# Kernel tuning notes

Hardware: AMD Instinct MI355X
Metric: run time of the kernel (lower is better)

The kernel has to match this reference:

```python
import jax, jax.numpy as jnp
import numpy as np

B, S, E, ND = 4, 2048, 1024, 2


def setup_inputs() -> dict:
    key = jax.random.key(0)
    ks = jax.random.split(key, 10)
    def lin_w(k, out_f, in_f):
        return (jax.random.normal(k, (out_f, in_f), jnp.float32) / np.sqrt(in_f).astype(np.float32))
    inp = {}
    inp["x"] = jax.random.normal(ks[0], (B, S, E), jnp.float32)
    inp["tfidf_scores"] = jax.random.uniform(ks[1], (B, S), jnp.float32)
    names = ["q_f", "k_f", "v_f", "q_b", "k_b", "v_b"]
    for i, n in enumerate(names):
        inp["W" + n] = lin_w(ks[2 + i], ND * E, E)
        inp["b" + n] = jnp.zeros((ND * E,), jnp.float32)
    inp["Wo"] = lin_w(ks[8], E, ND * E)
    inp["bo"] = jnp.zeros((E,), jnp.float32)
    return inp


def _proj(x, W, b):
    # Linear(E -> ND*E) then reshape to (B, S, ND, E)
    y = jnp.einsum('bse,fe->bsf', x, W) + b
    return y.reshape(x.shape[0], x.shape[1], ND, E)


def _attend(q, k, v, tfidf):
    # q,k,v: (B, S, ND, E); tfidf: (B, S) weights keys
    scale = 1.0 / jnp.sqrt(jnp.asarray(E, q.dtype))
    scores = jnp.einsum('bsde,btde->bdst', q, k) * scale
    scores = scores * tfidf[:, None, None, :]
    attn = jax.nn.softmax(scores, axis=-1)
    return jnp.einsum('bdst,btde->bsde', attn, v)


def reference(x, tfidf_scores, Wq_f, bq_f, Wk_f, bk_f, Wv_f, bv_f,
              Wq_b, bq_b, Wk_b, bk_b, Wv_b, bv_b, Wo, bo):
    # forward direction
    qf = _proj(x, Wq_f, bq_f)
    kf = _proj(x, Wk_f, bk_f)
    vf = _proj(x, Wv_f, bv_f)
    out_f = _attend(qf, kf, vf, tfidf_scores)
    # backward direction: reversed sequence
    xr = x[:, ::-1]
    tr = tfidf_scores[:, ::-1]
    qb = _proj(xr, Wq_b, bq_b)
    kb = _proj(xr, Wk_b, bk_b)
    vb = _proj(xr, Wv_b, bv_b)
    out_b = _attend(qb, kb, vb, tr)[:, ::-1]
    comb = (out_f + out_b).reshape(x.shape[0], x.shape[1], ND * E)
    return jnp.einsum('bsf,ef->bse', comb, Wo) + bo
```

## Files before the change

### kernel.cpp

```cpp
#include <hip/hip_runtime.h>
#include <hip/hip_bf16.h>
#include <stdint.h>

#define SEQ 2048
#define EMB 1024

typedef __attribute__((ext_vector_type(4))) float f32x4;
typedef __attribute__((ext_vector_type(8))) __bf16 bf16x8v;
typedef __attribute__((ext_vector_type(8))) unsigned short u16x8;
typedef __attribute__((ext_vector_type(4))) unsigned short u16x4;

static __device__ __forceinline__ float bf2f(unsigned short u){
  union { unsigned int i; float f; } v; v.i = ((unsigned int)u) << 16; return v.f;
}
static __device__ __forceinline__ unsigned short f2bf(float f){
  union { float f; unsigned int i; } v; v.f = f;
  unsigned int r = v.i + 0x7FFFu + ((v.i >> 16) & 1u);
  return (unsigned short)(r >> 16);
}

static __device__ __forceinline__ void gload16(const unsigned short* g, unsigned short* l){
  __builtin_amdgcn_global_load_lds(
      (__attribute__((address_space(1))) unsigned int*)(g),
      (__attribute__((address_space(3))) unsigned int*)(l), 16, 0, 0);
}

static __device__ __forceinline__ int xcd_swz(int bid, int nwg){
  int q = nwg >> 3;
  return (bid & 7) * q + (bid >> 3);
}

__global__ __launch_bounds__(256) void k_cvt_bf16(const float* __restrict__ in,
                                                  unsigned short* __restrict__ out, long n4){
  long i = (long)blockIdx.x * 256 + threadIdx.x;
  if (i >= n4) return;
  float4 v = ((const float4*)in)[i];
  u16x4 o; o.x = f2bf(v.x); o.y = f2bf(v.y); o.z = f2bf(v.z); o.w = f2bf(v.w);
  ((u16x4*)out)[i] = o;
}

__global__ __launch_bounds__(256) void k_build_wcat(
    const float* __restrict__ w0, const float* __restrict__ w1,
    const float* __restrict__ w2, const float* __restrict__ w3,
    const float* __restrict__ w4, const float* __restrict__ w5,
    unsigned short* __restrict__ wcat){
  long i = (long)blockIdx.x * 256 + threadIdx.x;
  long g = i * 4;
  int m = (int)(g >> 21);
  const float* src = (m==0)?w0:(m==1)?w1:(m==2)?w2:(m==3)?w3:(m==4)?w4:w5;
  long loc = g & ((1L<<21)-1);
  float4 v = *(const float4*)&src[loc];
  u16x4 o; o.x=f2bf(v.x); o.y=f2bf(v.y); o.z=f2bf(v.z); o.w=f2bf(v.w);
  *(u16x4*)&wcat[g] = o;
}

__global__ __launch_bounds__(256) void k_build_bcat(
    const float* b0, const float* b1, const float* b2,
    const float* b3, const float* b4, const float* b5, float* __restrict__ bcat){
  int i = blockIdx.x * 256 + threadIdx.x;
  int m = i >> 11;
  const float* src = (m==0)?b0:(m==1)?b1:(m==2)?b2:(m==3)?b3:(m==4)?b4:b5;
  bcat[i] = src[i & 2047];
}

#define M_LIN   0
#define M_SCORE 1
#define M_PV    2
#define M_OUT   3

template<int MODE, int BN>
__global__ __launch_bounds__(512, 2)
void gemm8(const unsigned short* __restrict__ A_,
           const unsigned short* __restrict__ B_,
           unsigned short* __restrict__ Cb, float* __restrict__ Cf,
           const float* __restrict__ bias, const float* __restrict__ tfb,
           int ld, int ldc, int tilesN, int accflag)
{
  constexpr int KD  = (MODE==M_PV || MODE==M_OUT) ? 2048 : 1024;
  constexpr int NT  = KD/64;
  constexpr int NREP= BN/64;
  constexpr int NLO = NREP/2;
  constexpr int GB  = BN/64;

  __shared__ __attribute__((aligned(16))) unsigned short As[2][256*64];
  __shared__ __attribute__((aligned(16))) unsigned short Bs[2][BN*64];

  const int tid = threadIdx.x;
  const int lane = tid & 63, wid = tid >> 6;
  const int wr = wid >> 2, wc = wid & 3;

  const int tile = xcd_swz(blockIdx.x, gridDim.x);
  const int tm = tile / tilesN, tn = tile % tilesN;
  const int y  = blockIdx.y;

  const unsigned short *A0 = A_, *B0 = B_;
  unsigned short* Cbp = Cb;
  float* Cfp = Cf;
  const float* trow = nullptr;

  if constexpr (MODE==M_SCORE) {
    const int bl = y >> 1, d = y & 1;
    A0 = A_ + (size_t)bl*SEQ*ld + d*1024;
    B0 = A0 + 2048;
    Cbp = Cb + (size_t)y*SEQ*SEQ;
    trow = tfb + (size_t)bl*SEQ;
  } else if constexpr (MODE==M_PV) {
    A0 = A_ + (size_t)y*SEQ*SEQ;
    B0 = B_ + (size_t)y*EMB*SEQ;
    Cbp = Cb + (size_t)(y>>1)*SEQ*2048 + (y&1)*1024;
  }

  const int sr = tid >> 3, ss = tid & 7;
  const int swz = (ss ^ (sr & 7)) * 8;
  const long tmrow = (long)tm*256, tncol = (long)tn*BN;
  const int lrow = lane & 15, lks = lane >> 4;

  const unsigned short* gA = A0 + (size_t)(tmrow + sr)*ld + swz;
  const unsigned short* gB = B0 + (size_t)(tncol + sr)*ld + swz;

  f32x4 acc[8][NREP];
  #pragma unroll
  for (int m=0;m<8;++m)
    #pragma unroll
    for (int n=0;n<NREP;++n)
      #pragma unroll
      for (int r=0;r<4;++r) acc[m][n][r] = 0.f;

#define STAGE(nb_, t_) { \
    const long ko_ = (long)(t_)*64; \
    _Pragma("unroll") \
    for (int p=0;p<4;++p) \
      gload16(gA + (size_t)(p*64)*ld + ko_, &As[nb_][p*4096 + tid*8]); \
    _Pragma("unroll") \
    for (int p=0;p<GB;++p) \
      gload16(gB + (size_t)(p*64)*ld + ko_, &Bs[nb_][p*4096 + tid*8]); }

#define LDA_F(dst, mh) { \
    _Pragma("unroll") \
    for (int m=0;m<4;++m){ \
      int row_ = (m + 4*(mh))*32 + wr*16 + lrow; \
      _Pragma("unroll") \
      for (int kk=0;kk<2;++kk){ \
        int slot_ = (kk*4 + lks) ^ (row_ & 7); \
        dst[m*2+kk] = *(const bf16x8v*)&As[buf][row_*64 + slot_*8]; \
      } } }

#define LDB_F(dst, nh) { \
    _Pragma("unroll") \
    for (int n=0;n<NLO;++n){ \
      int row_ = (n + NLO*(nh))*64 + wc*16 + lrow; \
      _Pragma("unroll") \
      for (int kk=0;kk<2;++kk){ \
        int slot_ = (kk*4 + lks) ^ (row_ & 7); \
        dst[n*2+kk] = *(const bf16x8v*)&Bs[buf][row_*64 + slot_*8]; \
      } } }

#define MMAC(mh, bfrag, nh) { \
    __builtin_amdgcn_s_setprio(1); \
    _Pragma("unroll") \
    for (int m=0;m<4;++m) \
      _Pragma("unroll") \
      for (int n=0;n<NLO;++n) \
        _Pragma("unroll") \
        for (int kk=0;kk<2;++kk) \
          acc[(mh)*4+m][(nh)*NLO+n] = __builtin_amdgcn_mfma_f32_16x16x32_bf16( \
              aF[m*2+kk], bfrag[n*2+kk], acc[(mh)*4+m][(nh)*NLO+n], 0,0,0); \
    __builtin_amdgcn_s_setprio(0); }

#define TILE_BODY() { \
    bf16x8v aF[8], bL[2*NLO], bH[2*NLO]; \
    LDA_F(aF, 0); \
    LDB_F(bL, 0); \
    MMAC(0, bL, 0); \
    LDB_F(bH, 1); \
    MMAC(0, bH, 1); \
    LDA_F(aF, 1); \
    MMAC(1, bH, 1); \
    MMAC(1, bL, 0); }

  STAGE(0, 0);
  __syncthreads();

  for (int t = 0; t < NT-1; ++t) {
    const int buf = t & 1;
    STAGE(buf ^ 1, t+1);
    TILE_BODY();
    __syncthreads();
  }
  {
    const int buf = (NT-1) & 1;
    TILE_BODY();
  }

  const int rr = (lane >> 4) * 4, cc = lane & 15;
  #pragma unroll
  for (int n=0;n<NREP;++n) {
    const long col = tncol + n*64 + wc*16 + cc;
    float cmul = 1.f, cadd = 0.f;
    if constexpr (MODE==M_SCORE) cmul = 0.03125f * trow[col];
    if constexpr (MODE==M_LIN)   cadd = bias[col];
    if constexpr (MODE==M_OUT)   cadd = bias[col];
    #pragma unroll
    for (int m=0;m<8;++m) {
      const long row = tmrow + m*32 + wr*16 + rr;
      #pragma unroll
      for (int r=0;r<4;++r) {
        float v = acc[m][n][r];
        if constexpr (MODE==M_SCORE) v *= cmul;
        else v += cadd;
        if constexpr (MODE==M_OUT) {
          Cfp[(row + r)*ldc + col] = v;
        } else if constexpr (MODE==M_PV) {
          size_t idx = (row + r)*(size_t)ldc + col;
          float w = v + (accflag ? bf2f(Cbp[idx]) : 0.f);
          Cbp[idx] = f2bf(w);
        } else {
          Cbp[(row + r)*(size_t)ldc + col] = f2bf(v);
        }
      }
    }
  }
#undef STAGE
#undef LDA_F
#undef LDB_F
#undef MMAC
#undef TILE_BODY
}

__global__ __launch_bounds__(256) void k_softmax(unsigned short* __restrict__ Sc){
  long row = blockIdx.x;
  unsigned short* p = Sc + row*SEQ + threadIdx.x*8;
  u16x8 raw = *(const u16x8*)p;
  float v[8]; float mx = -3.0e38f;
  #pragma unroll
  for (int j=0;j<8;++j){ v[j] = bf2f(raw[j]); mx = fmaxf(mx, v[j]); }
  #pragma unroll
  for (int o=1;o<64;o<<=1) mx = fmaxf(mx, __shfl_xor(mx, o));
  __shared__ float redm[4], reds[4];
  int wid = threadIdx.x >> 6, lane = threadIdx.x & 63;
  if (lane == 0) redm[wid] = mx;
  __syncthreads();
  mx = fmaxf(fmaxf(redm[0],redm[1]), fmaxf(redm[2],redm[3]));
  float s = 0.f;
  #pragma unroll
  for (int j=0;j<8;++j){ v[j] = __expf(v[j]-mx); s += v[j]; }
  #pragma unroll
  for (int o=1;o<64;o<<=1) s += __shfl_xor(s, o);
  if (lane == 0) reds[wid] = s;
  __syncthreads();
  s = reds[0]+reds[1]+reds[2]+reds[3];
  float inv = 1.0f / s;
  u16x8 outv;
  #pragma unroll
  for (int j=0;j<8;++j) outv[j] = f2bf(v[j]*inv);
  *(u16x8*)p = outv;
}

__global__ __launch_bounds__(256) void k_transpose_v(const unsigned short* __restrict__ Vsrc,
                                                     unsigned short* __restrict__ VT, int ld){
  __shared__ unsigned short tile[64][72];
  int y = blockIdx.y; int bl = y >> 1, d = y & 1;
  int tt = (blockIdx.x & 31) * 64;
  int te = (blockIdx.x >> 5) * 64;
  const unsigned short* src = Vsrc + (size_t)bl*SEQ*ld + d*1024;
  int tid = threadIdx.x;
  #pragma unroll
  for (int it=0; it<2; ++it){
    int c = it*256 + tid;
    int r = c >> 3, c8 = (c & 7) * 8;
    u16x8 v = *(const u16x8*)&src[(size_t)(tt + r)*ld + te + c8];
    *(u16x8*)&tile[r][c8] = v;
  }
  __syncthreads();
  #pragma unroll
  for (int it=0; it<2; ++it){
    int c = it*256 + tid;
    int re = c >> 3, c8 = (c & 7) * 8;
    u16x8 o;
    #pragma unroll
    for (int j=0;j<8;++j) o[j] = tile[c8 + j][re];
    *(u16x8*)&VT[((size_t)y*EMB + te + re)*SEQ + tt + c8] = o;
  }
}

extern "C" void kernel_launch(void* const* d_in, const int* in_sizes, int n_in,
                              void* d_out, int out_size, void* d_ws, size_t ws_size,
                              hipStream_t stream){
  const float* x  = (const float*)d_in[0];
  const float* tf = (const float*)d_in[1];
  const float* W[6]; const float* bz[6];
  for (int i=0;i<6;++i){ W[i]=(const float*)d_in[2+2*i]; bz[i]=(const float*)d_in[3+2*i]; }
  const float* Wo = (const float*)d_in[14];
  const float* bo = (const float*)d_in[15];
  float* outp = (float*)d_out;

  auto al = [](size_t b){ return (b + 255) & ~(size_t)255; };
  const size_t SZ_XB   = (size_t)8192*1024*2;
  const size_t SZ_WCAT = (size_t)12288*1024*2;
  const size_t SZ_WOB  = (size_t)1024*2048*2;
  const size_t SZ_BCAT = (size_t)12288*4;
  const size_t SZ_AO   = (size_t)8192*2048*2;
  const size_t fixedB  = al(SZ_XB)+al(SZ_WCAT)+al(SZ_WOB)+al(SZ_BCAT)+al(SZ_AO);

  auto chB = [&](int CB, bool merged)->size_t {
    return al((size_t)CB*SEQ*(merged?12288:6144)*2)
         + al((size_t)CB*2*SEQ*SEQ*2)
         + al((size_t)CB*2*EMB*SEQ*2);
  };
  int CB; bool merged;
  if      (ws_size >= fixedB + chB(2,true))  { CB=2; merged=true;  }
  else if (ws_size >= fixedB + chB(2,false)) { CB=2; merged=false; }
  else if (ws_size >= fixedB + chB(1,false)) { CB=1; merged=false; }
  else return;
  const int ldY = merged ? 12288 : 6144;

  char* ws = (char*)d_ws; size_t off = 0;
  auto take = [&](size_t bytes)->char* { char* p = ws + off; off += al(bytes); return p; };
  unsigned short* xb   = (unsigned short*)take(SZ_XB);
  unsigned short* Wcat = (unsigned short*)take(SZ_WCAT);
  unsigned short* WoB  = (unsigned short*)take(SZ_WOB);
  float*          bcat = (float*)take(SZ_BCAT);
  unsigned short* AO   = (unsigned short*)take(SZ_AO);
  unsigned short* Ych  = (unsigned short*)take((size_t)CB*SEQ*ldY*2);
  unsigned short* Sc   = (unsigned short*)take((size_t)CB*2*SEQ*SEQ*2);
  unsigned short* VT   = (unsigned short*)take((size_t)CB*2*EMB*SEQ*2);

  k_cvt_bf16   <<<8192, 256, 0, stream>>>(x, xb, 2097152);
  k_build_wcat <<<12288,256, 0, stream>>>(W[0],W[1],W[2],W[3],W[4],W[5], Wcat);
  k_cvt_bf16   <<<2048, 256, 0, stream>>>(Wo, WoB, 524288);
  k_build_bcat <<<48,   256, 0, stream>>>(bz[0],bz[1],bz[2],bz[3],bz[4],bz[5], bcat);

  for (int c = 0; c < 4/CB; ++c) {
    const int b0 = c*CB;
    const unsigned short* xchunk = xb + (size_t)b0*SEQ*1024;
    if (merged) {
      gemm8<M_LIN,256><<<dim3(CB*8*48, 1), 512, 0, stream>>>(
          xchunk, Wcat, Ych, nullptr, bcat, nullptr, 1024, 12288, 48, 0);
    }
    for (int dir = 0; dir < 2; ++dir) {
      const unsigned short* Ybase = Ych + (merged ? dir*6144 : 0);
      if (!merged) {
        gemm8<M_LIN,256><<<dim3(CB*8*24, 1), 512, 0, stream>>>(
            xchunk, Wcat + (size_t)dir*6144*1024, Ych, nullptr,
            bcat + dir*6144, nullptr, 1024, 6144, 24, 0);
      }
      gemm8<M_SCORE,256><<<dim3(64, 2*CB), 512, 0, stream>>>(
          Ybase, nullptr, Sc, nullptr, nullptr, tf + (size_t)b0*SEQ,
          ldY, 2048, 8, 0);
      k_softmax    <<<2*CB*SEQ, 256, 0, stream>>>(Sc);
      k_transpose_v<<<dim3(512, 2*CB), 256, 0, stream>>>(Ybase + 4096, VT, ldY);
      gemm8<M_PV,128><<<dim3(64, 2*CB), 512, 0, stream>>>(
          Sc, VT, AO + (size_t)b0*SEQ*2048, nullptr, nullptr, nullptr,
          2048, 2048, 8, dir);
    }
  }
  gemm8<M_OUT,128><<<dim3(256, 1), 512, 0, stream>>>(
      AO, WoB, nullptr, outp, bo, nullptr, 2048, 1024, 8, 0);
}
```

Measured before the change: 764.6 us.

## Replace GEMM with triple-buffered 256x128 tile kernel using vmcnt-gated prefetch

Replaces the double-buffered GEMM template with a single 256x128 tile kernel that keeps three LDS stages in flight. It waits on vmcnt instead of a full __syncthreads, so global loads two K-steps ahead overlap compute. The wave layout changes from 2x4 to 4x2 with 64x64 per-wave sub-tiles. LIN and SCORE GEMMs, which previously used 256-wide N tiles, now launch twice as many blocks with smaller tiles, which lowers per-block register use but raises A-tile reloads. Only one barrier per iteration remains, so correctness depends on the three-buffer rotation preventing overwrite of the buffer being read.

```diff
diff --git a/kernel.cpp b/kernel.cpp
--- a/kernel.cpp
+++ b/kernel.cpp
@@ -68,26 +68,23 @@
 #define M_PV    2
 #define M_OUT   3
 
-template<int MODE, int BN>
+template<int MODE>
 __global__ __launch_bounds__(512, 2)
-void gemm8(const unsigned short* __restrict__ A_,
-           const unsigned short* __restrict__ B_,
-           unsigned short* __restrict__ Cb, float* __restrict__ Cf,
-           const float* __restrict__ bias, const float* __restrict__ tfb,
-           int ld, int ldc, int tilesN, int accflag)
+void gemm3p(const unsigned short* __restrict__ A_,
+            const unsigned short* __restrict__ B_,
+            unsigned short* __restrict__ Cb, float* __restrict__ Cf,
+            const float* __restrict__ bias, const float* __restrict__ tfb,
+            int ld, int ldc, int tilesN, int accflag)
 {
-  constexpr int KD  = (MODE==M_PV || MODE==M_OUT) ? 2048 : 1024;
-  constexpr int NT  = KD/64;
-  constexpr int NREP= BN/64;
-  constexpr int NLO = NREP/2;
-  constexpr int GB  = BN/64;
-
-  __shared__ __attribute__((aligned(16))) unsigned short As[2][256*64];
-  __shared__ __attribute__((aligned(16))) unsigned short Bs[2][BN*64];
+  constexpr int KD = (MODE==M_PV || MODE==M_OUT) ? 2048 : 1024;
+  constexpr int NT = KD/64;
+
+  __shared__ __attribute__((aligned(16))) unsigned short AsAll[3*256*64];
+  __shared__ __attribute__((aligned(16))) unsigned short BsAll[3*128*64];
 
   const int tid = threadIdx.x;
   const int lane = tid & 63, wid = tid >> 6;
-  const int wr = wid >> 2, wc = wid & 3;
+  const int wr = wid >> 1, wc = wid & 1;
 
   const int tile = xcd_swz(blockIdx.x, gridDim.x);
   const int tm = tile / tilesN, tn = tile % tilesN;
@@ -112,104 +109,101 @@
 
   const int sr = tid >> 3, ss = tid & 7;
   const int swz = (ss ^ (sr & 7)) * 8;
-  const long tmrow = (long)tm*256, tncol = (long)tn*BN;
+  const long tmrow = (long)tm*256, tncol = (long)tn*128;
   const int lrow = lane & 15, lks = lane >> 4;
 
   const unsigned short* gA = A0 + (size_t)(tmrow + sr)*ld + swz;
   const unsigned short* gB = B0 + (size_t)(tncol + sr)*ld + swz;
 
-  f32x4 acc[8][NREP];
-  #pragma unroll
-  for (int m=0;m<8;++m)
+  f32x4 acc[4][4];
+  #pragma unroll
+  for (int m=0;m<4;++m)
     #pragma unroll
-    for (int n=0;n<NREP;++n)
+    for (int n=0;n<4;++n)
       #pragma unroll
       for (int r=0;r<4;++r) acc[m][n][r] = 0.f;
 
-#define STAGE(nb_, t_) { \
+#define STAGE(bi_, t_) { \
+    unsigned short* as_ = &AsAll[(bi_)*16384]; \
+    unsigned short* bs_ = &BsAll[(bi_)*8192]; \
     const long ko_ = (long)(t_)*64; \
     _Pragma("unroll") \
     for (int p=0;p<4;++p) \
-      gload16(gA + (size_t)(p*64)*ld + ko_, &As[nb_][p*4096 + tid*8]); \
-    _Pragma("unroll") \
-    for (int p=0;p<GB;++p) \
-      gload16(gB + (size_t)(p*64)*ld + ko_, &Bs[nb_][p*4096 + tid*8]); }
-
-#define LDA_F(dst, mh) { \
+      gload16(gA + (size_t)(p*64)*ld + ko_, &as_[p*4096 + tid*8]); \
+    _Pragma("unroll") \
+    for (int p=0;p<2;++p) \
+      gload16(gB + (size_t)(p*64)*ld + ko_, &bs_[p*4096 + tid*8]); }
+
+#define TILE_BODY(bi_) { \
+    const unsigned short* as_ = &AsAll[(bi_)*16384]; \
+    const unsigned short* bs_ = &BsAll[(bi_)*8192]; \
+    bf16x8v a_[4][2], b_[4][2]; \
     _Pragma("unroll") \
     for (int m=0;m<4;++m){ \
-      int row_ = (m + 4*(mh))*32 + wr*16 + lrow; \
+      int row_ = wr*64 + m*16 + lrow; \
       _Pragma("unroll") \
       for (int kk=0;kk<2;++kk){ \
         int slot_ = (kk*4 + lks) ^ (row_ & 7); \
-        dst[m*2+kk] = *(const bf16x8v*)&As[buf][row_*64 + slot_*8]; \
-      } } }
-
-#define LDB_F(dst, nh) { \
-    _Pragma("unroll") \
-    for (int n=0;n<NLO;++n){ \
-      int row_ = (n + NLO*(nh))*64 + wc*16 + lrow; \
+        a_[m][kk] = *(const bf16x8v*)&as_[row_*64 + slot_*8]; \
+      } } \
+    _Pragma("unroll") \
+    for (int n=0;n<4;++n){ \
+      int row_ = wc*64 + n*16 + lrow; \
       _Pragma("unroll") \
       for (int kk=0;kk<2;++kk){ \
         int slot_ = (kk*4 + lks) ^ (row_ & 7); \
-        dst[n*2+kk] = *(const bf16x8v*)&Bs[buf][row_*64 + slot_*8]; \
-      } } }
-
-#define MMAC(mh, bfrag, nh) { \
+        b_[n][kk] = *(const bf16x8v*)&bs_[row_*64 + slot_*8]; \
+      } } \
     __builtin_amdgcn_s_setprio(1); \
     _Pragma("unroll") \
     for (int m=0;m<4;++m) \
       _Pragma("unroll") \
-      for (int n=0;n<NLO;++n) \
+      for (int n=0;n<4;++n) \
         _Pragma("unroll") \
         for (int kk=0;kk<2;++kk) \
-          acc[(mh)*4+m][(nh)*NLO+n] = __builtin_amdgcn_mfma_f32_16x16x32_bf16( \
-              aF[m*2+kk], bfrag[n*2+kk], acc[(mh)*4+m][(nh)*NLO+n], 0,0,0); \
+          acc[m][n] = __builtin_amdgcn_mfma_f32_16x16x32_bf16( \
+              a_[m][kk], b_[n][kk], acc[m][n], 0,0,0); \
     __builtin_amdgcn_s_setprio(0); }
 
-#define TILE_BODY() { \
-    bf16x8v aF[8], bL[2*NLO], bH[2*NLO]; \
-    LDA_F(aF, 0); \
-    LDB_F(bL, 0); \
-    MMAC(0, bL, 0); \
-    LDB_F(bH, 1); \
-    MMAC(0, bH, 1); \
-    LDA_F(aF, 1); \
-    MMAC(1, bH, 1); \
-    MMAC(1, bL, 0); }
+#define GATE(N_) { \
+    asm volatile("s_waitcnt vmcnt(" #N_ ")" ::: "memory"); \
+    __builtin_amdgcn_sched_barrier(0); \
+    __builtin_amdgcn_s_barrier(); \
+    __builtin_amdgcn_sched_barrier(0); }
 
   STAGE(0, 0);
-  __syncthreads();
-
+  STAGE(1, 1);
+
+  int buf = 0;
   for (int t = 0; t < NT-1; ++t) {
-    const int buf = t & 1;
-    STAGE(buf ^ 1, t+1);
-    TILE_BODY();
-    __syncthreads();
-  }
-  {
-    const int buf = (NT-1) & 1;
-    TILE_BODY();
-  }
+    GATE(6);
+    if (t + 2 < NT) {
+      int b2 = buf + 2; if (b2 >= 3) b2 -= 3;
+      STAGE(b2, t+2);
+    }
+    TILE_BODY(buf);
+    ++buf; if (buf == 3) buf = 0;
+  }
+  GATE(0);
+  TILE_BODY(buf);
 
   const int rr = (lane >> 4) * 4, cc = lane & 15;
   #pragma unroll
-  for (int n=0;n<NREP;++n) {
-    const long col = tncol + n*64 + wc*16 + cc;
+  for (int n=0;n<4;++n) {
+    const long col = tncol + wc*64 + n*16 + cc;
     float cmul = 1.f, cadd = 0.f;
     if constexpr (MODE==M_SCORE) cmul = 0.03125f * trow[col];
-    if constexpr (MODE==M_LIN)   cadd = bias[col];
-    if constexpr (MODE==M_OUT)   cadd = bias[col];
+    if constexpr (MODE==M_LIN || MODE==M_OUT) cadd = bias[col];
     #pragma unroll
-    for (int m=0;m<8;++m) {
-      const long row = tmrow + m*32 + wr*16 + rr;
+    for (int m=0;m<4;++m) {
+      const long row = tmrow + wr*64 + m*16 + rr;
       #pragma unroll
       for (int r=0;r<4;++r) {
         float v = acc[m][n][r];
         if constexpr (MODE==M_SCORE) v *= cmul;
         else v += cadd;
         if constexpr (MODE==M_OUT) {
-          Cfp[(row + r)*ldc + col] = v;
+          Cfp[(row + r)*(size_t)ldc + col] = v;
         } else if constexpr (MODE==M_PV) {
           size_t idx = (row + r)*(size_t)ldc + col;
           float w = v + (accflag ? bf2f(Cbp[idx]) : 0.f);
@@ -221,10 +215,8 @@
     }
   }
 #undef STAGE
-#undef LDA_F
-#undef LDB_F
-#undef MMAC
 #undef TILE_BODY
+#undef GATE
 }
 
 __global__ __launch_bounds__(256) void k_softmax(unsigned short* __restrict__ Sc){
@@ -334,26 +326,26 @@
     const int b0 = c*CB;
     const unsigned short* xchunk = xb + (size_t)b0*SEQ*1024;
     if (merged) {
-      gemm8<M_LIN,256><<<dim3(CB*8*48, 1), 512, 0, stream>>>(
-          xchunk, Wcat, Ych, nullptr, bcat, nullptr, 1024, 12288, 48, 0);
+      gemm3p<M_LIN><<<dim3(CB*8*96, 1), 512, 0, stream>>>(
+          xchunk, Wcat, Ych, nullptr, bcat, nullptr, 1024, 12288, 96, 0);
     }
     for (int dir = 0; dir < 2; ++dir) {
       const unsigned short* Ybase = Ych + (merged ? dir*6144 : 0);
       if (!merged) {
-        gemm8<M_LIN,256><<<dim3(CB*8*24, 1), 512, 0, stream>>>(
+        gemm3p<M_LIN><<<dim3(CB*8*48, 1), 512, 0, stream>>>(
             xchunk, Wcat + (size_t)dir*6144*1024, Ych, nullptr,
-            bcat + dir*6144, nullptr, 1024, 6144, 24, 0);
+            bcat + dir*6144, nullptr, 1024, 6144, 48, 0);
       }
-      gemm8<M_SCORE,256><<<dim3(64, 2*CB), 512, 0, stream>>>(
+      gemm3p<M_SCORE><<<dim3(8*16, 2*CB), 512, 0, stream>>>(
           Ybase, nullptr, Sc, nullptr, nullptr, tf + (size_t)b0*SEQ,
-          ldY, 2048, 8, 0);
+          ldY, 2048, 16, 0);
       k_softmax    <<<2*CB*SEQ, 256, 0, stream>>>(Sc);
       k_transpose_v<<<dim3(512, 2*CB), 256, 0, stream>>>(Ybase + 4096, VT, ldY);
-      gemm8<M_PV,128><<<dim3(64, 2*CB), 512, 0, stream>>>(
+      gemm3p<M_PV><<<dim3(8*8, 2*CB), 512, 0, stream>>>(
           Sc, VT, AO + (size_t)b0*SEQ*2048, nullptr, nullptr, nullptr,
           2048, 2048, 8, dir);
     }
   }
-  gemm8<M_OUT,128><<<dim3(256, 1), 512, 0, stream>>>(
+  gemm3p<M_OUT><<<dim3(32*8, 1), 512, 0, stream>>>(
       AO, WoB, nullptr, outp, bo, nullptr, 2048, 1024, 8, 0);
 }
```

New measurement: 833.2 us. 9.0% more time.

## Split GEMM tile staging into quarter loads gated by partial vmcnt barriers

Applied to the files above, without the earlier changes.

Breaks the per-K-tile global-to-LDS staging into four pieces (two A halves, two B halves) and interleaves them with the MFMA phases. Each phase waits on a partial vmcnt count plus a raw s_barrier instead of a full __syncthreads. The aim is to keep loads in flight across the compute phases and avoid full drains at tile boundaries. This relies on hand-counted vmcnt values, so a miscount could cause races or stalls.

```diff
diff --git a/kernel.cpp b/kernel.cpp
--- a/kernel.cpp
+++ b/kernel.cpp
@@ -70,17 +70,17 @@
 
 template<int MODE, int BN>
 __global__ __launch_bounds__(512, 2)
-void gemm8(const unsigned short* __restrict__ A_,
-           const unsigned short* __restrict__ B_,
-           unsigned short* __restrict__ Cb, float* __restrict__ Cf,
-           const float* __restrict__ bias, const float* __restrict__ tfb,
-           int ld, int ldc, int tilesN, int accflag)
+void gemm4p(const unsigned short* __restrict__ A_,
+            const unsigned short* __restrict__ B_,
+            unsigned short* __restrict__ Cb, float* __restrict__ Cf,
+            const float* __restrict__ bias, const float* __restrict__ tfb,
+            int ld, int ldc, int tilesN, int accflag)
 {
   constexpr int KD  = (MODE==M_PV || MODE==M_OUT) ? 2048 : 1024;
   constexpr int NT  = KD/64;
   constexpr int NREP= BN/64;
   constexpr int NLO = NREP/2;
-  constexpr int GB  = BN/64;
+  constexpr int LB  = BN/128;
 
   __shared__ __attribute__((aligned(16))) unsigned short As[2][256*64];
   __shared__ __attribute__((aligned(16))) unsigned short Bs[2][BN*64];
@@ -126,33 +126,40 @@
       #pragma unroll
       for (int r=0;r<4;++r) acc[m][n][r] = 0.f;
 
-#define STAGE(nb_, t_) { \
+#define SA_H(b_, h_, t_) { \
     const long ko_ = (long)(t_)*64; \
     _Pragma("unroll") \
-    for (int p=0;p<4;++p) \
-      gload16(gA + (size_t)(p*64)*ld + ko_, &As[nb_][p*4096 + tid*8]); \
-    _Pragma("unroll") \
-    for (int p=0;p<GB;++p) \
-      gload16(gB + (size_t)(p*64)*ld + ko_, &Bs[nb_][p*4096 + tid*8]); }
-
-#define LDA_F(dst, mh) { \
+    for (int p=0;p<2;++p){ \
+      const int p2_ = (h_)*2 + p; \
+      gload16(gA + (size_t)(p2_*64)*ld + ko_, &As[b_][p2_*4096 + tid*8]); \
+    } }
+
+#define SB_H(b_, h_, t_) { \
+    const long ko_ = (long)(t_)*64; \
+    _Pragma("unroll") \
+    for (int p=0;p<LB;++p){ \
+      const int p2_ = (h_)*LB + p; \
+      gload16(gB + (size_t)(p2_*64)*ld + ko_, &Bs[b_][p2_*4096 + tid*8]); \
+    } }
+
+#define LDA_F(dst, b_, mh) { \
     _Pragma("unroll") \
     for (int m=0;m<4;++m){ \
       int row_ = (m + 4*(mh))*32 + wr*16 + lrow; \
       _Pragma("unroll") \
       for (int kk=0;kk<2;++kk){ \
         int slot_ = (kk*4 + lks) ^ (row_ & 7); \
-        dst[m*2+kk] = *(const bf16x8v*)&As[buf][row_*64 + slot_*8]; \
+        dst[m*2+kk] = *(const bf16x8v*)&As[b_][row_*64 + slot_*8]; \
       } } }
 
-#define LDB_F(dst, nh) { \
+#define LDB_F(dst, b_, nh) { \
     _Pragma("unroll") \
     for (int n=0;n<NLO;++n){ \
       int row_ = (n + NLO*(nh))*64 + wc*16 + lrow; \
       _Pragma("unroll") \
       for (int kk=0;kk<2;++kk){ \
         int slot_ = (kk*4 + lks) ^ (row_ & 7); \
-        dst[n*2+kk] = *(const bf16x8v*)&Bs[buf][row_*64 + slot_*8]; \
+        dst[n*2+kk] = *(const bf16x8v*)&Bs[b_][row_*64 + slot_*8]; \
       } } }
 
 #define MMAC(mh, bfrag, nh) { \
@@ -167,29 +174,48 @@
               aF[m*2+kk], bfrag[n*2+kk], acc[(mh)*4+m][(nh)*NLO+n], 0,0,0); \
     __builtin_amdgcn_s_setprio(0); }
 
-#define TILE_BODY() { \
-    bf16x8v aF[8], bL[2*NLO], bH[2*NLO]; \
-    LDA_F(aF, 0); \
-    LDB_F(bL, 0); \
-    MMAC(0, bL, 0); \
-    LDB_F(bH, 1); \
-    MMAC(0, bH, 1); \
-    LDA_F(aF, 1); \
-    MMAC(1, bH, 1); \
-    MMAC(1, bL, 0); }
-
-  STAGE(0, 0);
-  __syncthreads();
+#define GATEN(N_) { \
+    asm volatile("s_waitcnt vmcnt(" #N_ ")" ::: "memory"); \
+    __builtin_amdgcn_sched_barrier(0); \
+    __builtin_amdgcn_s_barrier(); \
+    __builtin_amdgcn_sched_barrier(0); }
+
+  SA_H(0,0,0); SB_H(0,0,0); SB_H(0,1,0); SA_H(0,1,0);
+
+  bf16x8v aF[8], bL[2*NLO], bH[2*NLO];
 
   for (int t = 0; t < NT-1; ++t) {
-    const int buf = t & 1;
-    STAGE(buf ^ 1, t+1);
-    TILE_BODY();
-    __syncthreads();
-  }
+    const int b_ = t & 1, nb_ = b_ ^ 1;
+    SA_H(nb_,0,t+1);
+    if constexpr (LB==2) { GATEN(6) } else { GATEN(5) }
+    LDA_F(aF, b_, 0);
+    LDB_F(bL, b_, 0);
+    MMAC(0, bL, 0);
+    SB_H(nb_,0,t+1);
+    if constexpr (LB==2) { GATEN(6) } else { GATEN(5) }
+    LDB_F(bH, b_, 1);
+    MMAC(0, bH, 1);
+    SB_H(nb_,1,t+1);
+    if constexpr (LB==2) { GATEN(6) } else { GATEN(4) }
+    LDA_F(aF, b_, 1);
+    MMAC(1, bH, 1);
+    SA_H(nb_,1,t+1);
+    MMAC(1, bL, 0);
+  }
+
   {
-    const int buf = (NT-1) & 1;
-    TILE_BODY();
+    const int b_ = (NT-1) & 1;
+    if constexpr (LB==2) { GATEN(4) } else { GATEN(3) }
+    LDA_F(aF, b_, 0);
+    LDB_F(bL, b_, 0);
+    MMAC(0, bL, 0);
+    GATEN(2)
+    LDB_F(bH, b_, 1);
+    MMAC(0, bH, 1);
+    GATEN(0)
+    LDA_F(aF, b_, 1);
+    MMAC(1, bH, 1);
+    MMAC(1, bL, 0);
   }
 
   const int rr = (lane >> 4) * 4, cc = lane & 15;
@@ -198,8 +224,7 @@
     const long col = tncol + n*64 + wc*16 + cc;
     float cmul = 1.f, cadd = 0.f;
     if constexpr (MODE==M_SCORE) cmul = 0.03125f * trow[col];
-    if constexpr (MODE==M_LIN)   cadd = bias[col];
-    if constexpr (MODE==M_OUT)   cadd = bias[col];
+    if constexpr (MODE==M_LIN || MODE==M_OUT) cadd = bias[col];
     #pragma unroll
     for (int m=0;m<8;++m) {
       const long row = tmrow + m*32 + wr*16 + rr;
@@ -209,7 +234,7 @@
         if constexpr (MODE==M_SCORE) v *= cmul;
         else v += cadd;
         if constexpr (MODE==M_OUT) {
-          Cfp[(row + r)*ldc + col] = v;
+          Cfp[(row + r)*(size_t)ldc + col] = v;
         } else if constexpr (MODE==M_PV) {
           size_t idx = (row + r)*(size_t)ldc + col;
           float w = v + (accflag ? bf2f(Cbp[idx]) : 0.f);
@@ -220,11 +245,12 @@
       }
     }
   }
-#undef STAGE
+#undef SA_H
+#undef SB_H
 #undef LDA_F
 #undef LDB_F
 #undef MMAC
-#undef TILE_BODY
+#undef GATEN
 }
 
 __global__ __launch_bounds__(256) void k_softmax(unsigned short* __restrict__ Sc){
@@ -334,26 +360,26 @@
     const int b0 = c*CB;
     const unsigned short* xchunk = xb + (size_t)b0*SEQ*1024;
     if (merged) {
-      gemm8<M_LIN,256><<<dim3(CB*8*48, 1), 512, 0, stream>>>(
+      gemm4p<M_LIN,256><<<dim3(CB*8*48, 1), 512, 0, stream>>>(
           xchunk, Wcat, Ych, nullptr, bcat, nullptr, 1024, 12288, 48, 0);
     }
     for (int dir = 0; dir < 2; ++dir) {
       const unsigned short* Ybase = Ych + (merged ? dir*6144 : 0);
       if (!merged) {
-        gemm8<M_LIN,256><<<dim3(CB*8*24, 1), 512, 0, stream>>>(
+        gemm4p<M_LIN,256><<<dim3(CB*8*24, 1), 512, 0, stream>>>(
             xchunk, Wcat + (size_t)dir*6144*1024, Ych, nullptr,
             bcat + dir*6144, nullptr, 1024, 6144, 24, 0);
       }
-      gemm8<M_SCORE,256><<<dim3(64, 2*CB), 512, 0, stream>>>(
+      gemm4p<M_SCORE,256><<<dim3(64, 2*CB), 512, 0, stream>>>(
           Ybase, nullptr, Sc, nullptr, nullptr, tf + (size_t)b0*SEQ,
           ldY, 2048, 8, 0);
       k_softmax    <<<2*CB*SEQ, 256, 0, stream>>>(Sc);
       k_transpose_v<<<dim3(512, 2*CB), 256, 0, stream>>>(Ybase + 4096, VT, ldY);
-      gemm8<M_PV,128><<<dim3(64, 2*CB), 512, 0, stream>>>(
+      gemm4p<M_PV,128><<<dim3(64, 2*CB), 512, 0, stream>>>(
           Sc, VT, AO + (size_t)b0*SEQ*2048, nullptr, nullptr, nullptr,
           2048, 2048, 8, dir);
     }
   }
-  gemm8<M_OUT,128><<<dim3(256, 1), 512, 0, stream>>>(
+  gemm4p<M_OUT,128><<<dim3(256, 1), 512, 0, stream>>>(
       AO, WoB, nullptr, outp, bo, nullptr, 2048, 1024, 8, 0);
 }
```

Measured after the change: 761.9 us. About the same (-0.4%).
